# Kernel optimization log

Hardware: AMD Instinct MI355X
Metric: run time of the kernel (lower is better)

The kernel has to match this reference:

```python
import jax, jax.numpy as jnp
import numpy as np

B, N, D = 4, 1024, 128  # batch, seq_len, embed_dim


def setup_inputs() -> dict:
    key = jax.random.key(0)
    ks = jax.random.split(key, 4)
    scale = 1.0 / np.sqrt(D)
    return {
        "inputs": jax.random.normal(ks[0], (B, N, D), dtype=jnp.float32),
        "Wq": jax.random.normal(ks[1], (D, D), dtype=jnp.float32) * scale,
        "bq": jnp.zeros((D,), dtype=jnp.float32),
        "Wk": jax.random.normal(ks[2], (D, D), dtype=jnp.float32) * scale,
        "bk": jnp.zeros((D,), dtype=jnp.float32),
        "Wv": jax.random.normal(ks[3], (D, D), dtype=jnp.float32) * scale,
        "bv": jnp.zeros((D,), dtype=jnp.float32),
    }


def reference(inputs, Wq, bq, Wk, bk, Wv, bv):
    # Dense projections (TF Dense: x @ W + b)
    q = inputs @ Wq + bq  # [B,N,D]
    k = inputs @ Wk + bk  # [B,N,D]
    v = inputs @ Wv + bv  # [B,N,D]
    # Original TF code:
    #   score   = einsum('bnd,bmd->bnmd', q, k)        (outer product per dim)
    #   weights = softmax(score, axis=2)               (computed but UNUSED --
    #                                                    call() returns attention built
    #                                                    from `score`, not `weights`)
    #   output  = einsum('bnmd,bmd->bnd', score, v)
    # Since score[b,n,m,d] = q[b,n,d]*k[b,m,d], the output factorizes exactly:
    #   output[b,n,d] = q[b,n,d] * sum_m k[b,m,d]*v[b,m,d]
    # This is the same math without materializing the O(N*M*D) tensor.
    kv = jnp.sum(k * v, axis=1, keepdims=True)  # [B,1,D]
    return q * kv  # [B,N,D]
```

## Files before the change

kernel.cpp:

```cpp
#include <hip/hip_runtime.h>


#define NN 1024
#define DD 128
#define MAGICPAIR 0x5EEDBEEFA5F00D1Eull

typedef __attribute__((ext_vector_type(8))) short short8;
typedef __attribute__((ext_vector_type(4))) float f32x4;

union Frag { short8 s; unsigned int u[4]; };

static __device__ __forceinline__ unsigned int cvtpk(float a, float b) {
    unsigned int r;
    asm("v_cvt_pk_bf16_f32 %0, %1, %2" : "=v"(r) : "v"(a), "v"(b));
    return r;
}

static __device__ __forceinline__ void split2(float a, float b,
                                              unsigned int& hp, unsigned int& lp) {
    hp = cvtpk(a, b);
    const float ha = __uint_as_float(hp << 16);
    const float hb = __uint_as_float(hp & 0xFFFF0000u);
    lp = cvtpk(a - ha, b - hb);
}

__global__ __launch_bounds__(512, 2) void fused_kernel(
    const float* __restrict__ x,
    const float* __restrict__ Wq, const float* __restrict__ bq,
    const float* __restrict__ Wk, const float* __restrict__ bk,
    const float* __restrict__ Wv, const float* __restrict__ bv,
    float* __restrict__ out, float* __restrict__ ws)
{
    __shared__ __align__(16) unsigned short xh[64][DD];
    __shared__ __align__(16) unsigned short xl[64][DD];
    __shared__ __align__(16) unsigned short wt[3][2][32][DD];
    __shared__ float red[4][32];
    __shared__ float kvs[32];

    const int bid = blockIdx.x;
    const int rt  = bid & 63;
    const int cgi = bid >> 6;
    const int tid = threadIdx.x;
    const int cbase = cgi << 5;
    const int b = rt >> 4;

    unsigned long long* flags64 = reinterpret_cast<unsigned long long*>(ws);
    float* partials = ws + 512;

    float4 xr[4];
    {
        const float4* src = reinterpret_cast<const float4*>(x + (size_t)rt * 64 * DD);
#pragma unroll
        for (int j = 0; j < 4; ++j) xr[j] = src[tid + j * 512];
    }

    {
        const int col = tid & 31;
        const int ko  = (tid >> 5) & 15;
        const int swz = (ko ^ (col & 7)) << 4;
#pragma unroll
        for (int m = 0; m < 3; ++m) {
            const float* wp = m == 0 ? Wq : (m == 1 ? Wk : Wv);
            const float* src = wp + (size_t)(ko << 3) * DD + cbase + col;
            float e[8];
#pragma unroll
            for (int i = 0; i < 8; ++i) e[i] = src[(size_t)i * DD];
            unsigned int hp[4], lp[4];
#pragma unroll
            for (int j = 0; j < 4; ++j) split2(e[2*j], e[2*j+1], hp[j], lp[j]);
            *reinterpret_cast<int4*>((char*)&wt[m][0][col][0] + swz) =
                *reinterpret_cast<int4*>(hp);
            *reinterpret_cast<int4*>((char*)&wt[m][1][col][0] + swz) =
                *reinterpret_cast<int4*>(lp);
        }
    }

    {
#pragma unroll
        for (int j = 0; j < 4; ++j) {
            const int idx = tid + j * 512;
            const float4 v = xr[j];
            const int row = idx >> 5, c4 = idx & 31;
            const int s = c4 >> 1, half = c4 & 1;
            const int off = ((s ^ (row & 7)) << 4) + (half << 3);
            unsigned int h0, l0, h1, l1;
            split2(v.x, v.y, h0, l0);
            split2(v.z, v.w, h1, l1);
            const unsigned long long hp =
                (unsigned long long)h0 | ((unsigned long long)h1 << 32);
            const unsigned long long lp =
                (unsigned long long)l0 | ((unsigned long long)l1 << 32);
            *reinterpret_cast<unsigned long long*>((char*)&xh[row][0] + off) = hp;
            *reinterpret_cast<unsigned long long*>((char*)&xl[row][0] + off) = lp;
        }
    }
    __syncthreads();

    const int lane  = tid & 63;
    const int w8    = tid >> 6;
    const int wr    = w8 >> 1;
    const int wc    = w8 & 1;
    const int lr    = lane & 15;
    const int kslot = lane >> 4;
    const int arow  = (wr << 4) + lr;
    const int bcol  = (wc << 4) + lr;

    f32x4 qa = {0.f, 0.f, 0.f, 0.f};
    f32x4 ka = {0.f, 0.f, 0.f, 0.f};
    f32x4 va = {0.f, 0.f, 0.f, 0.f};

    const char* xhp = (const char*)&xh[arow][0];
    const char* xlp = (const char*)&xl[arow][0];
    const int   aswz = arow & 7;
    const char* wb   = (const char*)&wt[0][0][bcol][0];
    const int   bswz = bcol & 7;
    const int   MATS = 2 * 32 * DD * 2;
    const int   HS   = 32 * DD * 2;

    Frag ah[4], al[4];

#pragma unroll
    for (int ks = 0; ks < 4; ++ks) {
        const int s   = (ks << 2) + kslot;
        const int aof = (s ^ aswz) << 4;
        const int bof = (s ^ bswz) << 4;
        Frag kh, kl, vh, vl;
        ah[ks].s = *reinterpret_cast<const short8*>(xhp + aof);
        al[ks].s = *reinterpret_cast<const short8*>(xlp + aof);
        kh.s = *reinterpret_cast<const short8*>(wb + MATS + bof);
        kl.s = *reinterpret_cast<const short8*>(wb + MATS + HS + bof);
        vh.s = *reinterpret_cast<const short8*>(wb + 2 * MATS + bof);
        vl.s = *reinterpret_cast<const short8*>(wb + 2 * MATS + HS + bof);

        ka = __builtin_amdgcn_mfma_f32_16x16x32_bf16(ah[ks].s, kh.s, ka, 0, 0, 0);
        ka = __builtin_amdgcn_mfma_f32_16x16x32_bf16(al[ks].s, kh.s, ka, 0, 0, 0);
        ka = __builtin_amdgcn_mfma_f32_16x16x32_bf16(ah[ks].s, kl.s, ka, 0, 0, 0);

        va = __builtin_amdgcn_mfma_f32_16x16x32_bf16(ah[ks].s, vh.s, va, 0, 0, 0);
        va = __builtin_amdgcn_mfma_f32_16x16x32_bf16(al[ks].s, vh.s, va, 0, 0, 0);
        va = __builtin_amdgcn_mfma_f32_16x16x32_bf16(ah[ks].s, vl.s, va, 0, 0, 0);
    }

    const int colg = cbase + (wc << 4) + lr;
    const float bqc = bq[colg], bkc = bk[colg], bvc = bv[colg];

    float p = 0.f;
#pragma unroll
    for (int i = 0; i < 4; ++i)
        p += (ka[i] + bkc) * (va[i] + bvc);
    p += __shfl_xor(p, 16);
    p += __shfl_xor(p, 32);
    if (lane < 16) red[wr][(wc << 4) + lane] = p;
    __syncthreads();

    if (tid < 32) {
        const float s = red[0][tid] + red[1][tid] + red[2][tid] + red[3][tid];
        __hip_atomic_store(&partials[(size_t)rt * DD + cbase + tid], s,
                           __ATOMIC_RELAXED, __HIP_MEMORY_SCOPE_AGENT);
    }
    __syncthreads();

    if (tid == 0)
        __hip_atomic_store(&flags64[bid], (unsigned long long)MAGICPAIR,
                           __ATOMIC_RELAXED, __HIP_MEMORY_SCOPE_AGENT);

#pragma unroll
    for (int ks = 0; ks < 4; ++ks) {
        const int s   = (ks << 2) + kslot;
        const int bof = (s ^ bswz) << 4;
        Frag qh, ql;
        qh.s = *reinterpret_cast<const short8*>(wb + bof);
        ql.s = *reinterpret_cast<const short8*>(wb + HS + bof);
        qa = __builtin_amdgcn_mfma_f32_16x16x32_bf16(ah[ks].s, qh.s, qa, 0, 0, 0);
        qa = __builtin_amdgcn_mfma_f32_16x16x32_bf16(al[ks].s, qh.s, qa, 0, 0, 0);
        qa = __builtin_amdgcn_mfma_f32_16x16x32_bf16(ah[ks].s, ql.s, qa, 0, 0, 0);
    }

    if (tid < 16) {
        const int wbid = (cgi << 6) + (b << 4) + tid;
        while (__hip_atomic_load(&flags64[wbid], __ATOMIC_RELAXED,
                                 __HIP_MEMORY_SCOPE_AGENT)
               != (unsigned long long)MAGICPAIR)
            __builtin_amdgcn_s_sleep(1);
    }
    __syncthreads();

    {
        float* scratch = reinterpret_cast<float*>(&xh[0][0]);
        const int col = tid & 31, rr = tid >> 5;
        const float pv = __hip_atomic_load(
            &partials[(size_t)((b << 4) + rr) * DD + cbase + col],
            __ATOMIC_RELAXED, __HIP_MEMORY_SCOPE_AGENT);
        scratch[rr * 32 + col] = pv;
        __syncthreads();
        if (tid < 32) {
            float s = 0.f;
#pragma unroll
            for (int j = 0; j < 16; ++j) s += scratch[j * 32 + tid];
            kvs[tid] = s;
        }
        __syncthreads();
    }

    const float kvc = kvs[(wc << 4) + lr];
    const size_t rbase = ((size_t)rt * 64 + (wr << 4) + (kslot << 2)) * DD + colg;
#pragma unroll
    for (int i = 0; i < 4; ++i)
        out[rbase + (size_t)i * DD] = (qa[i] + bqc) * kvc;
}

extern "C" void kernel_launch(void* const* d_in, const int* in_sizes, int n_in,
                              void* d_out, int out_size, void* d_ws, size_t ws_size,
                              hipStream_t stream) {
    const float* x  = (const float*)d_in[0];
    const float* Wq = (const float*)d_in[1];
    const float* bq = (const float*)d_in[2];
    const float* Wk = (const float*)d_in[3];
    const float* bk = (const float*)d_in[4];
    const float* Wv = (const float*)d_in[5];
    const float* bv = (const float*)d_in[6];
    float* out      = (float*)d_out;
    float* ws       = (float*)d_ws;

    fused_kernel<<<dim3(256), dim3(512), 0, stream>>>(
        x, Wq, bq, Wk, bk, Wv, bv, out, ws);
}
```

Baseline: 10.28 us.

## Double block size and split Q projection onto dedicated warps

Blocks grow from 512 to 1024 threads. Eight warps compute the K and V projections and the kv partials, while the other eight warps compute the Q projection at the same time. Before, one set of warps did K/V and then Q one after the other. This shortens the serial MFMA chain on each block's critical path before the cross-block spin wait, at the cost of larger blocks that may limit occupancy and of all blocks needing to be co-resident for the flag-based sync.

```diff
diff --git a/kernel.cpp b/kernel.cpp
--- a/kernel.cpp
+++ b/kernel.cpp
@@ -24,7 +24,7 @@
     lp = cvtpk(a - ha, b - hb);
 }
 
-__global__ __launch_bounds__(512, 2) void fused_kernel(
+__global__ __launch_bounds__(1024) void fused_kernel(
     const float* __restrict__ x,
     const float* __restrict__ Wq, const float* __restrict__ bq,
     const float* __restrict__ Wk, const float* __restrict__ bk,
@@ -47,67 +47,65 @@
     unsigned long long* flags64 = reinterpret_cast<unsigned long long*>(ws);
     float* partials = ws + 512;
 
-    float4 xr[4];
+    float4 xr[2];
     {
         const float4* src = reinterpret_cast<const float4*>(x + (size_t)rt * 64 * DD);
 #pragma unroll
-        for (int j = 0; j < 4; ++j) xr[j] = src[tid + j * 512];
-    }
-
-    {
-        const int col = tid & 31;
-        const int ko  = (tid >> 5) & 15;
-        const int swz = (ko ^ (col & 7)) << 4;
-#pragma unroll
-        for (int m = 0; m < 3; ++m) {
-            const float* wp = m == 0 ? Wq : (m == 1 ? Wk : Wv);
+        for (int j = 0; j < 2; ++j) xr[j] = src[tid + j * 1024];
+    }
+
+#pragma unroll
+    for (int j = 0; j < 2; ++j) {
+        const int u = tid + j * 1024;
+        if (j == 0 || tid < 512) {
+            const int col = u & 31;
+            const int ko  = (u >> 5) & 15;
+            const int mat = u >> 9;
+            const int swz = (ko ^ (col & 7)) << 4;
+            const float* wp = mat == 0 ? Wq : (mat == 1 ? Wk : Wv);
             const float* src = wp + (size_t)(ko << 3) * DD + cbase + col;
             float e[8];
 #pragma unroll
             for (int i = 0; i < 8; ++i) e[i] = src[(size_t)i * DD];
             unsigned int hp[4], lp[4];
 #pragma unroll
-            for (int j = 0; j < 4; ++j) split2(e[2*j], e[2*j+1], hp[j], lp[j]);
-            *reinterpret_cast<int4*>((char*)&wt[m][0][col][0] + swz) =
+            for (int jj = 0; jj < 4; ++jj) split2(e[2*jj], e[2*jj+1], hp[jj], lp[jj]);
+            *reinterpret_cast<int4*>((char*)&wt[mat][0][col][0] + swz) =
                 *reinterpret_cast<int4*>(hp);
-            *reinterpret_cast<int4*>((char*)&wt[m][1][col][0] + swz) =
+            *reinterpret_cast<int4*>((char*)&wt[mat][1][col][0] + swz) =
                 *reinterpret_cast<int4*>(lp);
         }
     }
 
-    {
-#pragma unroll
-        for (int j = 0; j < 4; ++j) {
-            const int idx = tid + j * 512;
-            const float4 v = xr[j];
-            const int row = idx >> 5, c4 = idx & 31;
-            const int s = c4 >> 1, half = c4 & 1;
-            const int off = ((s ^ (row & 7)) << 4) + (half << 3);
-            unsigned int h0, l0, h1, l1;
-            split2(v.x, v.y, h0, l0);
-            split2(v.z, v.w, h1, l1);
-            const unsigned long long hp =
-                (unsigned long long)h0 | ((unsigned long long)h1 << 32);
-            const unsigned long long lp =
-                (unsigned long long)l0 | ((unsigned long long)l1 << 32);
-            *reinterpret_cast<unsigned long long*>((char*)&xh[row][0] + off) = hp;
-            *reinterpret_cast<unsigned long long*>((char*)&xl[row][0] + off) = lp;
-        }
+#pragma unroll
+    for (int j = 0; j < 2; ++j) {
+        const int idx = tid + j * 1024;
+        const float4 v = xr[j];
+        const int row = idx >> 5, c4 = idx & 31;
+        const int s = c4 >> 1, half = c4 & 1;
+        const int off = ((s ^ (row & 7)) << 4) + (half << 3);
+        unsigned int h0, l0, h1, l1;
+        split2(v.x, v.y, h0, l0);
+        split2(v.z, v.w, h1, l1);
+        const unsigned long long hp =
+            (unsigned long long)h0 | ((unsigned long long)h1 << 32);
+        const unsigned long long lp =
+            (unsigned long long)l0 | ((unsigned long long)l1 << 32);
+        *reinterpret_cast<unsigned long long*>((char*)&xh[row][0] + off) = hp;
+        *reinterpret_cast<unsigned long long*>((char*)&xl[row][0] + off) = lp;
     }
     __syncthreads();
 
     const int lane  = tid & 63;
-    const int w8    = tid >> 6;
-    const int wr    = w8 >> 1;
-    const int wc    = w8 & 1;
+    const int w16   = tid >> 6;
+    const int isq   = w16 >> 3;
+    const int wsub  = w16 & 7;
+    const int wr    = wsub >> 1;
+    const int wc    = wsub & 1;
     const int lr    = lane & 15;
     const int kslot = lane >> 4;
     const int arow  = (wr << 4) + lr;
     const int bcol  = (wc << 4) + lr;
-
-    f32x4 qa = {0.f, 0.f, 0.f, 0.f};
-    f32x4 ka = {0.f, 0.f, 0.f, 0.f};
-    f32x4 va = {0.f, 0.f, 0.f, 0.f};
 
     const char* xhp = (const char*)&xh[arow][0];
     const char* xlp = (const char*)&xl[arow][0];
@@ -117,40 +115,58 @@
     const int   MATS = 2 * 32 * DD * 2;
     const int   HS   = 32 * DD * 2;
 
-    Frag ah[4], al[4];
-
-#pragma unroll
-    for (int ks = 0; ks < 4; ++ks) {
-        const int s   = (ks << 2) + kslot;
-        const int aof = (s ^ aswz) << 4;
-        const int bof = (s ^ bswz) << 4;
-        Frag kh, kl, vh, vl;
-        ah[ks].s = *reinterpret_cast<const short8*>(xhp + aof);
-        al[ks].s = *reinterpret_cast<const short8*>(xlp + aof);
-        kh.s = *reinterpret_cast<const short8*>(wb + MATS + bof);
-        kl.s = *reinterpret_cast<const short8*>(wb + MATS + HS + bof);
-        vh.s = *reinterpret_cast<const short8*>(wb + 2 * MATS + bof);
-        vl.s = *reinterpret_cast<const short8*>(wb + 2 * MATS + HS + bof);
-
-        ka = __builtin_amdgcn_mfma_f32_16x16x32_bf16(ah[ks].s, kh.s, ka, 0, 0, 0);
-        ka = __builtin_amdgcn_mfma_f32_16x16x32_bf16(al[ks].s, kh.s, ka, 0, 0, 0);
-        ka = __builtin_amdgcn_mfma_f32_16x16x32_bf16(ah[ks].s, kl.s, ka, 0, 0, 0);
-
-        va = __builtin_amdgcn_mfma_f32_16x16x32_bf16(ah[ks].s, vh.s, va, 0, 0, 0);
-        va = __builtin_amdgcn_mfma_f32_16x16x32_bf16(al[ks].s, vh.s, va, 0, 0, 0);
-        va = __builtin_amdgcn_mfma_f32_16x16x32_bf16(ah[ks].s, vl.s, va, 0, 0, 0);
-    }
-
     const int colg = cbase + (wc << 4) + lr;
-    const float bqc = bq[colg], bkc = bk[colg], bvc = bv[colg];
-
+
+    f32x4 qa = {0.f, 0.f, 0.f, 0.f};
     float p = 0.f;
-#pragma unroll
-    for (int i = 0; i < 4; ++i)
-        p += (ka[i] + bkc) * (va[i] + bvc);
-    p += __shfl_xor(p, 16);
-    p += __shfl_xor(p, 32);
-    if (lane < 16) red[wr][(wc << 4) + lane] = p;
+
+    if (!isq) {
+        f32x4 ka = {0.f, 0.f, 0.f, 0.f};
+        f32x4 va = {0.f, 0.f, 0.f, 0.f};
+#pragma unroll
+        for (int ks = 0; ks < 4; ++ks) {
+            const int s   = (ks << 2) + kslot;
+            const int aof = (s ^ aswz) << 4;
+            const int bof = (s ^ bswz) << 4;
+            Frag ah, al, kh, kl, vh, vl;
+            ah.s = *reinterpret_cast<const short8*>(xhp + aof);
+            al.s = *reinterpret_cast<const short8*>(xlp + aof);
+            kh.s = *reinterpret_cast<const short8*>(wb + MATS + bof);
+            kl.s = *reinterpret_cast<const short8*>(wb + MATS + HS + bof);
+            vh.s = *reinterpret_cast<const short8*>(wb + 2 * MATS + bof);
+            vl.s = *reinterpret_cast<const short8*>(wb + 2 * MATS + HS + bof);
+
+            ka = __builtin_amdgcn_mfma_f32_16x16x32_bf16(ah.s, kh.s, ka, 0, 0, 0);
+            ka = __builtin_amdgcn_mfma_f32_16x16x32_bf16(al.s, kh.s, ka, 0, 0, 0);
+            ka = __builtin_amdgcn_mfma_f32_16x16x32_bf16(ah.s, kl.s, ka, 0, 0, 0);
+
+            va = __builtin_amdgcn_mfma_f32_16x16x32_bf16(ah.s, vh.s, va, 0, 0, 0);
+            va = __builtin_amdgcn_mfma_f32_16x16x32_bf16(al.s, vh.s, va, 0, 0, 0);
+            va = __builtin_amdgcn_mfma_f32_16x16x32_bf16(ah.s, vl.s, va, 0, 0, 0);
+        }
+        const float bkc = bk[colg], bvc = bv[colg];
+#pragma unroll
+        for (int i = 0; i < 4; ++i)
+            p += (ka[i] + bkc) * (va[i] + bvc);
+        p += __shfl_xor(p, 16);
+        p += __shfl_xor(p, 32);
+        if (lane < 16) red[wr][(wc << 4) + lane] = p;
+    } else {
+#pragma unroll
+        for (int ks = 0; ks < 4; ++ks) {
+            const int s   = (ks << 2) + kslot;
+            const int aof = (s ^ aswz) << 4;
+            const int bof = (s ^ bswz) << 4;
+            Frag ah, al, qh, ql;
+            ah.s = *reinterpret_cast<const short8*>(xhp + aof);
+            al.s = *reinterpret_cast<const short8*>(xlp + aof);
+            qh.s = *reinterpret_cast<const short8*>(wb + bof);
+            ql.s = *reinterpret_cast<const short8*>(wb + HS + bof);
+            qa = __builtin_amdgcn_mfma_f32_16x16x32_bf16(ah.s, qh.s, qa, 0, 0, 0);
+            qa = __builtin_amdgcn_mfma_f32_16x16x32_bf16(al.s, qh.s, qa, 0, 0, 0);
+            qa = __builtin_amdgcn_mfma_f32_16x16x32_bf16(ah.s, ql.s, qa, 0, 0, 0);
+        }
+    }
     __syncthreads();
 
     if (tid < 32) {
@@ -163,18 +179,6 @@
     if (tid == 0)
         __hip_atomic_store(&flags64[bid], (unsigned long long)MAGICPAIR,
                            __ATOMIC_RELAXED, __HIP_MEMORY_SCOPE_AGENT);
-
-#pragma unroll
-    for (int ks = 0; ks < 4; ++ks) {
-        const int s   = (ks << 2) + kslot;
-        const int bof = (s ^ bswz) << 4;
-        Frag qh, ql;
-        qh.s = *reinterpret_cast<const short8*>(wb + bof);
-        ql.s = *reinterpret_cast<const short8*>(wb + HS + bof);
-        qa = __builtin_amdgcn_mfma_f32_16x16x32_bf16(ah[ks].s, qh.s, qa, 0, 0, 0);
-        qa = __builtin_amdgcn_mfma_f32_16x16x32_bf16(al[ks].s, qh.s, qa, 0, 0, 0);
-        qa = __builtin_amdgcn_mfma_f32_16x16x32_bf16(ah[ks].s, ql.s, qa, 0, 0, 0);
-    }
 
     if (tid < 16) {
         const int wbid = (cgi << 6) + (b << 4) + tid;
@@ -187,11 +191,13 @@
 
     {
         float* scratch = reinterpret_cast<float*>(&xh[0][0]);
-        const int col = tid & 31, rr = tid >> 5;
-        const float pv = __hip_atomic_load(
-            &partials[(size_t)((b << 4) + rr) * DD + cbase + col],
-            __ATOMIC_RELAXED, __HIP_MEMORY_SCOPE_AGENT);
-        scratch[rr * 32 + col] = pv;
+        if (tid < 512) {
+            const int col = tid & 31, rr = tid >> 5;
+            const float pv = __hip_atomic_load(
+                &partials[(size_t)((b << 4) + rr) * DD + cbase + col],
+                __ATOMIC_RELAXED, __HIP_MEMORY_SCOPE_AGENT);
+            scratch[rr * 32 + col] = pv;
+        }
         __syncthreads();
         if (tid < 32) {
             float s = 0.f;
@@ -202,11 +208,15 @@
         __syncthreads();
     }
 
-    const float kvc = kvs[(wc << 4) + lr];
-    const size_t rbase = ((size_t)rt * 64 + (wr << 4) + (kslot << 2)) * DD + colg;
-#pragma unroll
-    for (int i = 0; i < 4; ++i)
-        out[rbase + (size_t)i * DD] = (qa[i] + bqc) * kvc;
+    if (isq) {
+        const float bqc = bq[colg];
+        const float kvc = kvs[(wc << 4) + lr];
+        const size_t rbase =
+            ((size_t)rt * 64 + (wr << 4) + (kslot << 2)) * DD + colg;
+#pragma unroll
+        for (int i = 0; i < 4; ++i)
+            out[rbase + (size_t)i * DD] = (qa[i] + bqc) * kvc;
+    }
 }
 
 extern "C" void kernel_launch(void* const* d_in, const int* in_sizes, int n_in,
@@ -222,6 +232,6 @@
     float* out      = (float*)d_out;
     float* ws       = (float*)d_ws;
 
-    fused_kernel<<<dim3(256), dim3(512), 0, stream>>>(
+    fused_kernel<<<dim3(256), dim3(1024), 0, stream>>>(
         x, Wq, bq, Wk, bk, Wv, bv, out, ws);
 }
```

New measurement: 10.61 us. 1.03x slower.
